# Performance work log

Measured on AMD Instinct MI355X. Metric: run time of the kernel, lower is better.

Reference implementation:

```python
import jax, jax.numpy as jnp
import numpy as np

DC_WZ = 15
ETA = 0.1
RADIUS = DC_WZ // 2  # 7
EPS = 1e-3


def avg_pool2d(x, k, pad):
    # torch F.avg_pool2d default: zero padding, count_include_pad=True -> divide by k*k always
    s = jax.lax.reduce_window(
        x, 0.0, jax.lax.add,
        window_dimensions=(1, 1, k, k),
        window_strides=(1, 1, 1, 1),
        padding=[(0, 0), (0, 0), (pad, pad), (pad, pad)])
    return s / float(k * k)


def min_pool2d_replicate(x, k, pad):
    # replicate (edge) pad then VALID min-pool, matching -max_pool2d(-pad(x, replicate))
    xp = jnp.pad(x, ((0, 0), (0, 0), (pad, pad), (pad, pad)), mode='edge')
    return jax.lax.reduce_window(
        xp, jnp.inf, jax.lax.min,
        window_dimensions=(1, 1, k, k),
        window_strides=(1, 1, 1, 1),
        padding='VALID')


def guided_filter(guide, src, radius, eps=EPS):
    k = 2 * radius + 1
    mean_I = avg_pool2d(guide, k, radius)
    mean_p = avg_pool2d(src, k, radius)
    mean_Ip = avg_pool2d(guide * src, k, radius)
    cov_Ip = mean_Ip - mean_I * mean_p
    mean_II = avg_pool2d(guide * guide, k, radius)
    var_I = mean_II - mean_I * mean_I
    a = cov_Ip / (var_I + eps)
    b = mean_p - a * mean_I
    mean_a = avg_pool2d(a, k, radius)
    mean_b = avg_pool2d(b, k, radius)
    return mean_a * guide + mean_b


def setup_inputs() -> dict:
    key = jax.random.key(0)
    k1, k2 = jax.random.split(key)
    smoky_image = jax.random.uniform(k1, (16, 3, 512, 512), dtype=jnp.float32)
    rho_DNN = jax.random.uniform(k2, (16, 3, 512, 512), dtype=jnp.float32)
    return {"smoky_image": smoky_image, "rho_DNN": rho_DNN}


def reference(smoky_image, rho_DNN):
    # dark channel: per-pixel min over RGB, then 15x15 min-pool with replicate pad
    dc_pixel = jnp.min(smoky_image, axis=-3, keepdims=True)  # [B,1,H,W]
    dc_coarse = min_pool2d_replicate(dc_pixel, DC_WZ, RADIUS)
    guide_I = jnp.mean(smoky_image, axis=-3, keepdims=True)
    dc_refined = guided_filter(guide_I, dc_coarse, RADIUS, EPS)
    dc_refined = jax.lax.stop_gradient(dc_refined)  # torch: no_grad + detach
    dc_rho = (ETA + dc_refined) / (ETA + 1.0) * (1.0 - rho_DNN)
    return smoky_image - dc_rho
```

## Files before the change

### kernel.cpp

```cpp
#include <hip/hip_runtime.h>

#define BATCH 16
#define HH 512
#define WW 512
#define PLANE (HH*WW)

#define LDS_WAIT()   asm volatile("s_waitcnt lgkmcnt(0)" ::: "memory")
#define WAVE_FENCE() asm volatile("" ::: "memory")

__device__ __forceinline__ float bf_lo(unsigned u) {
    union { unsigned u; float f; } c; c.u = u << 16; return c.f;
}
__device__ __forceinline__ float bf_hi(unsigned u) {
    union { unsigned u; float f; } c; c.u = u & 0xFFFF0000u; return c.f;
}
__device__ __forceinline__ unsigned f2bf(float f) {
    union { float f; unsigned u; } c; c.f = f;
    return (c.u + 0x7FFFu + ((c.u >> 16) & 1u)) >> 16;
}
__device__ __forceinline__ unsigned packbf(float x, float y) {
    return f2bf(x) | (f2bf(y) << 16);
}
__device__ __forceinline__ float min3f(float a, float b, float c) {
    return fminf(fminf(a, b), c);
}

#define T1 64
#define HALO 7
#define LW (T1 + 2*HALO)

__global__ __launch_bounds__(256) void k1_guide_minpool(
    const float* __restrict__ smoky, unsigned* __restrict__ gp)
{
    __shared__ float dcp[LW*LW];
    __shared__ float vmn[T1*LW];
    __shared__ unsigned short gsh[T1*T1];
    int nwg = gridDim.x;
    int wg = (blockIdx.x & 7) * (nwg >> 3) + (blockIdx.x >> 3);
    int img  = wg >> 6;
    int tile = wg & 63;
    int y0 = (tile >> 3) * T1;
    int x0 = (tile & 7) * T1;
    int t = threadIdx.x;
    const float* s0 = smoky + (size_t)img * 3 * PLANE;
    unsigned* gpl = gp + (size_t)img * PLANE;

    for (int i = t; i < LW*LW; i += 256) {
        int ly = i / LW, lx = i - ly * LW;
        int iy = y0 - HALO + ly, ix = x0 - HALO + lx;
        int cy = min(max(iy, 0), HH-1);
        int cx = min(max(ix, 0), WW-1);
        const float* bp = s0 + cy * WW + cx;
        float c0 = bp[0], c1 = bp[PLANE], c2 = bp[2*PLANE];
        dcp[i] = min3f(c0, c1, c2);
        if (ly >= HALO && ly < HALO+T1 && lx >= HALO && lx < HALO+T1)
            gsh[(ly-HALO)*T1 + (lx-HALO)] = (unsigned short)f2bf((c0 + c1 + c2) * (1.0f/3.0f));
    }
    __syncthreads();
    for (int i = t; i < T1*LW; i += 256) {
        int r = i / LW, c = i - r * LW;
        const float* q = &dcp[r*LW + c];
        float m = min3f(min3f(min3f(q[0*LW],q[1*LW],q[2*LW]),
                              min3f(q[3*LW],q[4*LW],q[5*LW]),
                              min3f(q[6*LW],q[7*LW],q[8*LW])),
                        min3f(q[9*LW],q[10*LW],q[11*LW]),
                        min3f(q[12*LW],q[13*LW],q[14*LW]));
        vmn[i] = m;
    }
    __syncthreads();
    for (int i = t; i < T1*T1; i += 256) {
        int r = i >> 6, c = i & 63;
        const float* q = &vmn[r*LW + c];
        float m = min3f(min3f(min3f(q[0],q[1],q[2]),
                              min3f(q[3],q[4],q[5]),
                              min3f(q[6],q[7],q[8])),
                        min3f(q[9],q[10],q[11]),
                        min3f(q[12],q[13],q[14]));
        gpl[(y0+r)*WW + x0 + c] = (unsigned)gsh[r*T1+c] | (f2bf(m) << 16);
    }
}

#define RS2 16

#define TSUM15(Q) ( (((Q(0)+Q(1))+(Q(2)+Q(3))) + ((Q(4)+Q(5))+(Q(6)+Q(7)))) \
                  + (((Q(8)+Q(9))+(Q(10)+Q(11))) + ((Q(12)+Q(13))+Q(14))) )

__global__ __launch_bounds__(256) void k2_ab(
    const unsigned* __restrict__ gp, unsigned* __restrict__ abO)
{
    __shared__ float ls[4][4][80];
    int nwg = gridDim.x;
    int wg = (blockIdx.x & 7) * (nwg >> 3) + (blockIdx.x >> 3);
    int w = threadIdx.x >> 6, l = threadIdx.x & 63;
    int gw = wg * 4 + w;
    int img   = gw >> 8;
    int cg    = (gw >> 5) & 7;
    int strip = gw & 31;
    int y0 = strip * RS2;
    int c0 = cg * 64;
    const unsigned* gpP = gp + (size_t)img * PLANE;
    unsigned* abP = abO + (size_t)img * PLANE;

    int col0 = c0 - 7 + l;
    int col1 = c0 + 57 + l;
    bool v0 = (col0 >= 0);
    bool v1 = (l < 14) && (col1 < WW);

    float sI0=0,sII0=0,sP0=0,sIp0=0;
    float sI1=0,sII1=0,sP1=0,sIp1=0;

    auto loadrow = [&](int y, unsigned& u0, unsigned& u1) {
        int yc = min(max(y, 0), HH-1);
        const unsigned* r = gpP + (size_t)yc * WW;
        unsigned a = 0u, b = 0u;
        if (v0) a = r[col0];
        if (v1) b = r[col1];
        bool rv = ((unsigned)y < (unsigned)HH);
        u0 = rv ? a : 0u;
        u1 = rv ? b : 0u;
    };

    for (int r = y0 - 8; r <= y0 + 6; ++r) {
        unsigned u0,u1; loadrow(r, u0,u1);
        float g0=bf_lo(u0), p0=bf_hi(u0), g1=bf_lo(u1), p1=bf_hi(u1);
        sI0+=g0; sII0+=g0*g0; sP0+=p0; sIp0+=g0*p0;
        sI1+=g1; sII1+=g1*g1; sP1+=p1; sIp1+=g1*p1;
    }
    unsigned adA, adB, sbA, sbB;
    loadrow(y0 + 7, adA, adB);
    loadrow(y0 - 8, sbA, sbB);

    float* L = &ls[w][0][0];
    const float inv225 = 1.0f/225.0f;
    for (int y = y0; y < y0 + RS2; ++y) {
        {
            float gA0=bf_lo(adA), pA0=bf_hi(adA), gA1=bf_lo(adB), pA1=bf_hi(adB);
            float gS0=bf_lo(sbA), pS0=bf_hi(sbA), gS1=bf_lo(sbB), pS1=bf_hi(sbB);
            sI0 += gA0-gS0; sII0 += gA0*gA0-gS0*gS0; sP0 += pA0-pS0; sIp0 += gA0*pA0-gS0*pS0;
            sI1 += gA1-gS1; sII1 += gA1*gA1-gS1*gS1; sP1 += pA1-pS1; sIp1 += gA1*pA1-gS1*pS1;
        }
        loadrow(y + 8, adA, adB);
        loadrow(y - 7, sbA, sbB);
        L[l] = sI0; L[80+l] = sII0; L[160+l] = sP0; L[240+l] = sIp0;
        if (l < 14) { L[64+l] = sI1; L[144+l] = sII1; L[224+l] = sP1; L[304+l] = sIp1; }
        LDS_WAIT();
        #define QI(d)  L[l+(d)]
        #define QII(d) L[80+l+(d)]
        #define QP(d)  L[160+l+(d)]
        #define QIp(d) L[240+l+(d)]
        float SI  = TSUM15(QI);
        float SII = TSUM15(QII);
        float SP  = TSUM15(QP);
        float SIp = TSUM15(QIp);
        #undef QI
        #undef QII
        #undef QP
        #undef QIp
        WAVE_FENCE();
        float mI = SI*inv225, mP = SP*inv225;
        float va = (SIp*inv225 - mI*mP) / (SII*inv225 - mI*mI + 1e-3f);
        abP[(size_t)y*WW + c0 + l] = packbf(va, mP - va*mI);
    }
}

__global__ __launch_bounds__(256) void k3_final(
    const unsigned* __restrict__ abI,
    const float* __restrict__ smoky, const float* __restrict__ rho,
    float* __restrict__ out)
{
    __shared__ float ls[4][2][80];
    int nwg = gridDim.x;
    int wg = (blockIdx.x & 7) * (nwg >> 3) + (blockIdx.x >> 3);
    int w = threadIdx.x >> 6, l = threadIdx.x & 63;
    int gw = wg * 4 + w;
    int img   = gw >> 8;
    int cg    = (gw >> 5) & 7;
    int strip = gw & 31;
    int y0 = strip * RS2;
    int c0 = cg * 64;
    const unsigned* abP = abI + (size_t)img * PLANE;
    const float* sP = smoky + (size_t)img * 3 * PLANE;
    const float* rP = rho   + (size_t)img * 3 * PLANE;
    float* oP = out + (size_t)img * 3 * PLANE;

    int col0 = c0 - 7 + l;
    int col1 = c0 + 57 + l;
    bool v0 = (col0 >= 0);
    bool v1 = (l < 14) && (col1 < WW);

    float sa0=0, sb0=0, sa1=0, sb1=0;

    auto loadrow = [&](int y, unsigned& u0, unsigned& u1) {
        int yc = min(max(y, 0), HH-1);
        const unsigned* r = abP + (size_t)yc * WW;
        unsigned a = 0u, b = 0u;
        if (v0) a = r[col0];
        if (v1) b = r[col1];
        bool rv = ((unsigned)y < (unsigned)HH);
        u0 = rv ? a : 0u;
        u1 = rv ? b : 0u;
    };

    for (int r = y0 - 8; r <= y0 + 6; ++r) {
        unsigned u0,u1; loadrow(r, u0,u1);
        sa0 += bf_lo(u0); sb0 += bf_hi(u0);
        sa1 += bf_lo(u1); sb1 += bf_hi(u1);
    }
    unsigned adA, adB, sbA, sbB;
    loadrow(y0 + 7, adA, adB);
    loadrow(y0 - 8, sbA, sbB);

    float es0,es1,es2, er0,er1,er2;
    int yend = y0 + RS2;
    auto loademit = [&](int y) {
        int e = min(y, yend - 1);
        size_t off = (size_t)e*WW + c0 + l;
        es0 = sP[off]; es1 = sP[off+PLANE]; es2 = sP[off+2*PLANE];
        er0 = rP[off]; er1 = rP[off+PLANE]; er2 = rP[off+2*PLANE];
    };
    loademit(y0);

    float* L = &ls[w][0][0];
    const float inv225 = 1.0f/225.0f;
    const float inv11  = 1.0f/1.1f;
    const float third  = 1.0f/3.0f;
    for (int y = y0; y < yend; ++y) {
        sa0 += bf_lo(adA) - bf_lo(sbA);  sb0 += bf_hi(adA) - bf_hi(sbA);
        sa1 += bf_lo(adB) - bf_lo(sbB);  sb1 += bf_hi(adB) - bf_hi(sbB);
        float s0 = es0, s1 = es1, s2 = es2, r0 = er0, r1 = er1, r2 = er2;
        float g = (s0 + s1 + s2) * third;
        loadrow(y + 8, adA, adB);
        loadrow(y - 7, sbA, sbB);
        loademit(y + 1);
        L[l] = sa0; L[80+l] = sb0;
        if (l < 14) { L[64+l] = sa1; L[144+l] = sb1; }
        LDS_WAIT();
        #define QA(d) L[l+(d)]
        #define QB(d) L[80+l+(d)]
        float SA = TSUM15(QA);
        float SB = TSUM15(QB);
        #undef QA
        #undef QB
        WAVE_FENCE();
        float dcr = SA*inv225*g + SB*inv225;
        float f = (0.1f + dcr) * inv11;
        size_t off = (size_t)y*WW + c0 + l;
        oP[off]          = s0 - f*(1.0f - r0);
        oP[off+PLANE]    = s1 - f*(1.0f - r1);
        oP[off+2*PLANE]  = s2 - f*(1.0f - r2);
    }
}

extern "C" void kernel_launch(void* const* d_in, const int* in_sizes, int n_in,
                              void* d_out, int out_size, void* d_ws, size_t ws_size,
                              hipStream_t stream) {
    const float* smoky = (const float*)d_in[0];
    const float* rho   = (const float*)d_in[1];
    float* out = (float*)d_out;
    const size_t P = (size_t)BATCH * PLANE;
    unsigned* gpbuf = (unsigned*)d_ws;
    unsigned* abbuf = (unsigned*)d_ws + P;

    k1_guide_minpool<<<BATCH*64, 256, 0, stream>>>(smoky, gpbuf);
    k2_ab<<<BATCH*64, 256, 0, stream>>>(gpbuf, abbuf);
    k3_final<<<BATCH*64, 256, 0, stream>>>(abbuf, smoky, rho, out);
}
```

Measured before the change: 81.86 us.

## Process two columns per lane with float2 LDS even/odd box-sum sharing

k2 and k3 now give each lane two adjacent columns, so a wave covers 128 columns over 8-row strips instead of 64 columns over 16-row strips. Global loads and stores become 64-bit vectors. Running column sums are stored to LDS as float2 pairs, and the 15-wide horizontal sum for the second column is derived from the first by adding and subtracting one element. This cuts LDS reads, scalar memory instructions and halo overhead per pixel, in exchange for shorter strips that raise the relative cost of the 15-row vertical warm-up and for more registers per lane.

Result: no change. 81.38 us (-0.6%).

```diff
diff --git a/kernel.cpp b/kernel.cpp
--- a/kernel.cpp
+++ b/kernel.cpp
@@ -80,86 +80,112 @@
     }
 }
 
-#define RS2 16
-
-#define TSUM15(Q) ( (((Q(0)+Q(1))+(Q(2)+Q(3))) + ((Q(4)+Q(5))+(Q(6)+Q(7)))) \
-                  + (((Q(8)+Q(9))+(Q(10)+Q(11))) + ((Q(12)+Q(13))+Q(14))) )
+#define RS2 8
 
 __global__ __launch_bounds__(256) void k2_ab(
     const unsigned* __restrict__ gp, unsigned* __restrict__ abO)
 {
-    __shared__ float ls[4][4][80];
+    __shared__ float2 eo[4][4][80];
     int nwg = gridDim.x;
     int wg = (blockIdx.x & 7) * (nwg >> 3) + (blockIdx.x >> 3);
     int w = threadIdx.x >> 6, l = threadIdx.x & 63;
     int gw = wg * 4 + w;
     int img   = gw >> 8;
-    int cg    = (gw >> 5) & 7;
-    int strip = gw & 31;
+    int cg    = (gw >> 6) & 3;
+    int strip = gw & 63;
     int y0 = strip * RS2;
-    int c0 = cg * 64;
+    int c0 = cg * 128;
     const unsigned* gpP = gp + (size_t)img * PLANE;
     unsigned* abP = abO + (size_t)img * PLANE;
 
-    int col0 = c0 - 7 + l;
-    int col1 = c0 + 57 + l;
-    bool v0 = (col0 >= 0);
-    bool v1 = (l < 14) && (col1 < WW);
-
-    float sI0=0,sII0=0,sP0=0,sIp0=0;
-    float sI1=0,sII1=0,sP1=0,sIp1=0;
-
-    auto loadrow = [&](int y, unsigned& u0, unsigned& u1) {
+    int cm = c0 + 2*l;
+    int hj = l & 3;
+    int hcol  = (l < 4) ? (c0 - 8 + 2*hj) : (c0 + 128 + 2*hj);
+    bool hv   = (l < 8) && (hcol >= 0) && (hcol < WW);
+    int hslot = (l < 4) ? hj : (68 + hj);
+
+    float sI[2]={0,0}, sII[2]={0,0}, sPv[2]={0,0}, sIp[2]={0,0};
+    float hI[2]={0,0}, hII[2]={0,0}, hPv[2]={0,0}, hIp[2]={0,0};
+
+    auto loadrow = [&](int y, uint2& um, uint2& uh) {
         int yc = min(max(y, 0), HH-1);
         const unsigned* r = gpP + (size_t)yc * WW;
-        unsigned a = 0u, b = 0u;
-        if (v0) a = r[col0];
-        if (v1) b = r[col1];
+        uint2 a = *reinterpret_cast<const uint2*>(r + cm);
+        uint2 b = make_uint2(0u, 0u);
+        if (hv) b = *reinterpret_cast<const uint2*>(r + hcol);
         bool rv = ((unsigned)y < (unsigned)HH);
-        u0 = rv ? a : 0u;
-        u1 = rv ? b : 0u;
+        um.x = rv ? a.x : 0u;  um.y = rv ? a.y : 0u;
+        uh.x = rv ? b.x : 0u;  uh.y = rv ? b.y : 0u;
     };
 
     for (int r = y0 - 8; r <= y0 + 6; ++r) {
-        unsigned u0,u1; loadrow(r, u0,u1);
-        float g0=bf_lo(u0), p0=bf_hi(u0), g1=bf_lo(u1), p1=bf_hi(u1);
-        sI0+=g0; sII0+=g0*g0; sP0+=p0; sIp0+=g0*p0;
-        sI1+=g1; sII1+=g1*g1; sP1+=p1; sIp1+=g1*p1;
-    }
-    unsigned adA, adB, sbA, sbB;
-    loadrow(y0 + 7, adA, adB);
-    loadrow(y0 - 8, sbA, sbB);
-
-    float* L = &ls[w][0][0];
+        uint2 um, uh; loadrow(r, um, uh);
+        unsigned mm[2]={um.x,um.y}, hh[2]={uh.x,uh.y};
+        #pragma unroll
+        for (int k = 0; k < 2; ++k) {
+            float g=bf_lo(mm[k]), p=bf_hi(mm[k]);
+            sI[k]+=g; sII[k]+=g*g; sPv[k]+=p; sIp[k]+=g*p;
+            float gh=bf_lo(hh[k]), ph=bf_hi(hh[k]);
+            hI[k]+=gh; hII[k]+=gh*gh; hPv[k]+=ph; hIp[k]+=gh*ph;
+        }
+    }
+    uint2 adM, adH, sbM, sbH;
+    loadrow(y0 + 7, adM, adH);
+    loadrow(y0 - 8, sbM, sbH);
+
+    float2* EO = &eo[w][0][0];
     const float inv225 = 1.0f/225.0f;
     for (int y = y0; y < y0 + RS2; ++y) {
         {
-            float gA0=bf_lo(adA), pA0=bf_hi(adA), gA1=bf_lo(adB), pA1=bf_hi(adB);
-            float gS0=bf_lo(sbA), pS0=bf_hi(sbA), gS1=bf_lo(sbB), pS1=bf_hi(sbB);
-            sI0 += gA0-gS0; sII0 += gA0*gA0-gS0*gS0; sP0 += pA0-pS0; sIp0 += gA0*pA0-gS0*pS0;
-            sI1 += gA1-gS1; sII1 += gA1*gA1-gS1*gS1; sP1 += pA1-pS1; sIp1 += gA1*pA1-gS1*pS1;
-        }
-        loadrow(y + 8, adA, adB);
-        loadrow(y - 7, sbA, sbB);
-        L[l] = sI0; L[80+l] = sII0; L[160+l] = sP0; L[240+l] = sIp0;
-        if (l < 14) { L[64+l] = sI1; L[144+l] = sII1; L[224+l] = sP1; L[304+l] = sIp1; }
+            unsigned am[2]={adM.x,adM.y}, sm[2]={sbM.x,sbM.y};
+            unsigned ah[2]={adH.x,adH.y}, sh[2]={sbH.x,sbH.y};
+            #pragma unroll
+            for (int k = 0; k < 2; ++k) {
+                float gA=bf_lo(am[k]), pA=bf_hi(am[k]);
+                float gS=bf_lo(sm[k]), pS=bf_hi(sm[k]);
+                sI[k]+=gA-gS; sII[k]+=gA*gA-gS*gS; sPv[k]+=pA-pS; sIp[k]+=gA*pA-gS*pS;
+                float gAh=bf_lo(ah[k]), pAh=bf_hi(ah[k]);
+                float gSh=bf_lo(sh[k]), pSh=bf_hi(sh[k]);
+                hI[k]+=gAh-gSh; hII[k]+=gAh*gAh-gSh*gSh; hPv[k]+=pAh-pSh; hIp[k]+=gAh*pAh-gSh*pSh;
+            }
+        }
+        loadrow(y + 8, adM, adH);
+        loadrow(y - 7, sbM, sbH);
+        EO[l+4]       = make_float2(sI[0],  sI[1]);
+        EO[80 + l+4]  = make_float2(sII[0], sII[1]);
+        EO[160 + l+4] = make_float2(sPv[0], sPv[1]);
+        EO[240 + l+4] = make_float2(sIp[0], sIp[1]);
+        if (l < 8) {
+            EO[hslot]       = make_float2(hI[0],  hI[1]);
+            EO[80 + hslot]  = make_float2(hII[0], hII[1]);
+            EO[160 + hslot] = make_float2(hPv[0], hPv[1]);
+            EO[240 + hslot] = make_float2(hIp[0], hIp[1]);
+        }
         LDS_WAIT();
-        #define QI(d)  L[l+(d)]
-        #define QII(d) L[80+l+(d)]
-        #define QP(d)  L[160+l+(d)]
-        #define QIp(d) L[240+l+(d)]
-        float SI  = TSUM15(QI);
-        float SII = TSUM15(QII);
-        float SP  = TSUM15(QP);
-        float SIp = TSUM15(QIp);
-        #undef QI
-        #undef QII
-        #undef QP
-        #undef QIp
+        float S0[4], S1[4];
+        #pragma unroll
+        for (int q = 0; q < 4; ++q) {
+            float2 t[9];
+            #pragma unroll
+            for (int m = 0; m < 9; ++m) t[m] = EO[q*80 + l + m];
+            float so = ((t[0].y+t[1].y)+(t[2].y+t[3].y)) + ((t[4].y+t[5].y)+(t[6].y+t[7].y));
+            float se = ((t[1].x+t[2].x)+(t[3].x+t[4].x)) + ((t[5].x+t[6].x)+t[7].x);
+            S0[q] = so + se;
+            S1[q] = S0[q] - t[0].y + t[8].x;
+        }
         WAVE_FENCE();
-        float mI = SI*inv225, mP = SP*inv225;
-        float va = (SIp*inv225 - mI*mP) / (SII*inv225 - mI*mI + 1e-3f);
-        abP[(size_t)y*WW + c0 + l] = packbf(va, mP - va*mI);
+        unsigned pk0, pk1;
+        {
+            float mI = S0[0]*inv225, mP = S0[2]*inv225;
+            float va = (S0[3]*inv225 - mI*mP) / (S0[1]*inv225 - mI*mI + 1e-3f);
+            pk0 = packbf(va, mP - va*mI);
+        }
+        {
+            float mI = S1[0]*inv225, mP = S1[2]*inv225;
+            float va = (S1[3]*inv225 - mI*mP) / (S1[1]*inv225 - mI*mI + 1e-3f);
+            pk1 = packbf(va, mP - va*mI);
+        }
+        *reinterpret_cast<uint2*>(abP + (size_t)y*WW + cm) = make_uint2(pk0, pk1);
     }
 }
 
@@ -168,86 +194,115 @@
     const float* __restrict__ smoky, const float* __restrict__ rho,
     float* __restrict__ out)
 {
-    __shared__ float ls[4][2][80];
+    __shared__ float2 eo[4][2][80];
     int nwg = gridDim.x;
     int wg = (blockIdx.x & 7) * (nwg >> 3) + (blockIdx.x >> 3);
     int w = threadIdx.x >> 6, l = threadIdx.x & 63;
     int gw = wg * 4 + w;
     int img   = gw >> 8;
-    int cg    = (gw >> 5) & 7;
-    int strip = gw & 31;
+    int cg    = (gw >> 6) & 3;
+    int strip = gw & 63;
     int y0 = strip * RS2;
-    int c0 = cg * 64;
+    int c0 = cg * 128;
     const unsigned* abP = abI + (size_t)img * PLANE;
     const float* sP = smoky + (size_t)img * 3 * PLANE;
     const float* rP = rho   + (size_t)img * 3 * PLANE;
     float* oP = out + (size_t)img * 3 * PLANE;
 
-    int col0 = c0 - 7 + l;
-    int col1 = c0 + 57 + l;
-    bool v0 = (col0 >= 0);
-    bool v1 = (l < 14) && (col1 < WW);
-
-    float sa0=0, sb0=0, sa1=0, sb1=0;
-
-    auto loadrow = [&](int y, unsigned& u0, unsigned& u1) {
+    int cm = c0 + 2*l;
+    int hj = l & 3;
+    int hcol  = (l < 4) ? (c0 - 8 + 2*hj) : (c0 + 128 + 2*hj);
+    bool hv   = (l < 8) && (hcol >= 0) && (hcol < WW);
+    int hslot = (l < 4) ? hj : (68 + hj);
+
+    float sa[2]={0,0}, sb[2]={0,0}, ha[2]={0,0}, hb[2]={0,0};
+
+    auto loadrow = [&](int y, uint2& um, uint2& uh) {
         int yc = min(max(y, 0), HH-1);
         const unsigned* r = abP + (size_t)yc * WW;
-        unsigned a = 0u, b = 0u;
-        if (v0) a = r[col0];
-        if (v1) b = r[col1];
+        uint2 a = *reinterpret_cast<const uint2*>(r + cm);
+        uint2 b = make_uint2(0u, 0u);
+        if (hv) b = *reinterpret_cast<const uint2*>(r + hcol);
         bool rv = ((unsigned)y < (unsigned)HH);
-        u0 = rv ? a : 0u;
-        u1 = rv ? b : 0u;
+        um.x = rv ? a.x : 0u;  um.y = rv ? a.y : 0u;
+        uh.x = rv ? b.x : 0u;  uh.y = rv ? b.y : 0u;
     };
 
     for (int r = y0 - 8; r <= y0 + 6; ++r) {
-        unsigned u0,u1; loadrow(r, u0,u1);
-        sa0 += bf_lo(u0); sb0 += bf_hi(u0);
-        sa1 += bf_lo(u1); sb1 += bf_hi(u1);
-    }
-    unsigned adA, adB, sbA, sbB;
-    loadrow(y0 + 7, adA, adB);
-    loadrow(y0 - 8, sbA, sbB);
-
-    float es0,es1,es2, er0,er1,er2;
+        uint2 um, uh; loadrow(r, um, uh);
+        sa[0]+=bf_lo(um.x); sb[0]+=bf_hi(um.x);
+        sa[1]+=bf_lo(um.y); sb[1]+=bf_hi(um.y);
+        ha[0]+=bf_lo(uh.x); hb[0]+=bf_hi(uh.x);
+        ha[1]+=bf_lo(uh.y); hb[1]+=bf_hi(uh.y);
+    }
+    uint2 adM, adH, sbM, sbH;
+    loadrow(y0 + 7, adM, adH);
+    loadrow(y0 - 8, sbM, sbH);
+
+    float2 es0, es1, es2, er0, er1, er2;
     int yend = y0 + RS2;
     auto loademit = [&](int y) {
         int e = min(y, yend - 1);
-        size_t off = (size_t)e*WW + c0 + l;
-        es0 = sP[off]; es1 = sP[off+PLANE]; es2 = sP[off+2*PLANE];
-        er0 = rP[off]; er1 = rP[off+PLANE]; er2 = rP[off+2*PLANE];
+        size_t off = (size_t)e*WW + cm;
+        es0 = *reinterpret_cast<const float2*>(sP + off);
+        es1 = *reinterpret_cast<const float2*>(sP + off + PLANE);
+        es2 = *reinterpret_cast<const float2*>(sP + off + 2*PLANE);
+        er0 = *reinterpret_cast<const float2*>(rP + off);
+        er1 = *reinterpret_cast<const float2*>(rP + off + PLANE);
+        er2 = *reinterpret_cast<const float2*>(rP + off + 2*PLANE);
     };
     loademit(y0);
 
-    float* L = &ls[w][0][0];
+    float2* EO = &eo[w][0][0];
     const float inv225 = 1.0f/225.0f;
     const float inv11  = 1.0f/1.1f;
     const float third  = 1.0f/3.0f;
     for (int y = y0; y < yend; ++y) {
-        sa0 += bf_lo(adA) - bf_lo(sbA);  sb0 += bf_hi(adA) - bf_hi(sbA);
-        sa1 += bf_lo(adB) - bf_lo(sbB);  sb1 += bf_hi(adB) - bf_hi(sbB);
-        float s0 = es0, s1 = es1, s2 = es2, r0 = er0, r1 = er1, r2 = er2;
-        float g = (s0 + s1 + s2) * third;
-        loadrow(y + 8, adA, adB);
-        loadrow(y - 7, sbA, sbB);
+        sa[0] += bf_lo(adM.x) - bf_lo(sbM.x);  sb[0] += bf_hi(adM.x) - bf_hi(sbM.x);
+        sa[1] += bf_lo(adM.y) - bf_lo(sbM.y);  sb[1] += bf_hi(adM.y) - bf_hi(sbM.y);
+        ha[0] += bf_lo(adH.x) - bf_lo(sbH.x);  hb[0] += bf_hi(adH.x) - bf_hi(sbH.x);
+        ha[1] += bf_lo(adH.y) - bf_lo(sbH.y);  hb[1] += bf_hi(adH.y) - bf_hi(sbH.y);
+        float2 cs0 = es0, cs1 = es1, cs2 = es2, cr0 = er0, cr1 = er1, cr2 = er2;
+        loadrow(y + 8, adM, adH);
+        loadrow(y - 7, sbM, sbH);
         loademit(y + 1);
-        L[l] = sa0; L[80+l] = sb0;
-        if (l < 14) { L[64+l] = sa1; L[144+l] = sb1; }
+        EO[l+4]      = make_float2(sa[0], sa[1]);
+        EO[80 + l+4] = make_float2(sb[0], sb[1]);
+        if (l < 8) {
+            EO[hslot]      = make_float2(ha[0], ha[1]);
+            EO[80 + hslot] = make_float2(hb[0], hb[1]);
+        }
         LDS_WAIT();
-        #define QA(d) L[l+(d)]
-        #define QB(d) L[80+l+(d)]
-        float SA = TSUM15(QA);
-        float SB = TSUM15(QB);
-        #undef QA
-        #undef QB
+        float SA0, SA1, SB0, SB1;
+        {
+            float2 t[9];
+            #pragma unroll
+            for (int m = 0; m < 9; ++m) t[m] = EO[l + m];
+            float so = ((t[0].y+t[1].y)+(t[2].y+t[3].y)) + ((t[4].y+t[5].y)+(t[6].y+t[7].y));
+            float se = ((t[1].x+t[2].x)+(t[3].x+t[4].x)) + ((t[5].x+t[6].x)+t[7].x);
+            SA0 = so + se;  SA1 = SA0 - t[0].y + t[8].x;
+        }
+        {
+            float2 t[9];
+            #pragma unroll
+            for (int m = 0; m < 9; ++m) t[m] = EO[80 + l + m];
+            float so = ((t[0].y+t[1].y)+(t[2].y+t[3].y)) + ((t[4].y+t[5].y)+(t[6].y+t[7].y));
+            float se = ((t[1].x+t[2].x)+(t[3].x+t[4].x)) + ((t[5].x+t[6].x)+t[7].x);
+            SB0 = so + se;  SB1 = SB0 - t[0].y + t[8].x;
+        }
         WAVE_FENCE();
-        float dcr = SA*inv225*g + SB*inv225;
-        float f = (0.1f + dcr) * inv11;
-        size_t off = (size_t)y*WW + c0 + l;
-        oP[off]          = s0 - f*(1.0f - r0);
-        oP[off+PLANE]    = s1 - f*(1.0f - r1);
-        oP[off+2*PLANE]  = s2 - f*(1.0f - r2);
+        float g0 = (cs0.x + cs1.x + cs2.x) * third;
+        float g1 = (cs0.y + cs1.y + cs2.y) * third;
+        float f0 = (0.1f + SA0*inv225*g0 + SB0*inv225) * inv11;
+        float f1 = (0.1f + SA1*inv225*g1 + SB1*inv225) * inv11;
+        size_t off = (size_t)y*WW + cm;
+        float2 o0, o1, o2;
+        o0.x = cs0.x - f0*(1.0f - cr0.x);  o0.y = cs0.y - f1*(1.0f - cr0.y);
+        o1.x = cs1.x - f0*(1.0f - cr1.x);  o1.y = cs1.y - f1*(1.0f - cr1.y);
+        o2.x = cs2.x - f0*(1.0f - cr2.x);  o2.y = cs2.y - f1*(1.0f - cr2.y);
+        *reinterpret_cast<float2*>(oP + off)           = o0;
+        *reinterpret_cast<float2*>(oP + off + PLANE)   = o1;
+        *reinterpret_cast<float2*>(oP + off + 2*PLANE) = o2;
     }
 }
 
```

## Fuse a/b computation and final box-filter kernels with an LDS ring buffer

Applied to the files above, without the earlier changes.

Merges the k2 (a,b coefficient) and k3 (mean_a/mean_b plus output) kernels into one kernel. Each wave computes a,b for a widened column halo of 14 pixels per side and a 7-row vertical halo, and keeps them in a 16-row LDS ring buffer that feeds the second running box sum. This removes the intermediate a,b buffer's global write and read plus one launch. In exchange, the halo rows and columns of a,b are recomputed redundantly, there is more LDS traffic, and the emit pipeline gets longer.

After: 122.1 us. 1.49x slower.

```diff
diff --git a/kernel.cpp b/kernel.cpp
--- a/kernel.cpp
+++ b/kernel.cpp
@@ -80,15 +80,17 @@
     }
 }
 
-#define RS2 16
-
-#define TSUM15(Q) ( (((Q(0)+Q(1))+(Q(2)+Q(3))) + ((Q(4)+Q(5))+(Q(6)+Q(7)))) \
-                  + (((Q(8)+Q(9))+(Q(10)+Q(11))) + ((Q(12)+Q(13))+Q(14))) )
-
-__global__ __launch_bounds__(256) void k2_ab(
-    const unsigned* __restrict__ gp, unsigned* __restrict__ abO)
+#define RSF 16
+
+__global__ __launch_bounds__(256) void k23(
+    const unsigned* __restrict__ gp,
+    const float* __restrict__ smoky, const float* __restrict__ rho,
+    float* __restrict__ out)
 {
-    __shared__ float ls[4][4][80];
+    __shared__ float    ex1[4][384];
+    __shared__ unsigned ring[4][16][80];
+    __shared__ float2   ex2[4][80];
+
     int nwg = gridDim.x;
     int wg = (blockIdx.x & 7) * (nwg >> 3) + (blockIdx.x >> 3);
     int w = threadIdx.x >> 6, l = threadIdx.x & 63;
@@ -96,158 +98,138 @@
     int img   = gw >> 8;
     int cg    = (gw >> 5) & 7;
     int strip = gw & 31;
-    int y0 = strip * RS2;
+    int y0 = strip * RSF;
     int c0 = cg * 64;
+
     const unsigned* gpP = gp + (size_t)img * PLANE;
-    unsigned* abP = abO + (size_t)img * PLANE;
-
-    int col0 = c0 - 7 + l;
-    int col1 = c0 + 57 + l;
-    bool v0 = (col0 >= 0);
-    bool v1 = (l < 14) && (col1 < WW);
-
-    float sI0=0,sII0=0,sP0=0,sIp0=0;
-    float sI1=0,sII1=0,sP1=0,sIp1=0;
-
-    auto loadrow = [&](int y, unsigned& u0, unsigned& u1) {
+    const float* sP = smoky + (size_t)img * 3 * PLANE;
+    const float* rP = rho   + (size_t)img * 3 * PLANE;
+    float* oP = out + (size_t)img * 3 * PLANE;
+
+    int colA = c0 - 14 + l;
+    int colB = c0 + 50 + l;
+    bool vA = (colA >= 0);
+    bool vB = (l < 28) && (colB < WW);
+
+    auto loadgp = [&](int y, unsigned& u0, unsigned& u1) {
         int yc = min(max(y, 0), HH-1);
         const unsigned* r = gpP + (size_t)yc * WW;
         unsigned a = 0u, b = 0u;
-        if (v0) a = r[col0];
-        if (v1) b = r[col1];
+        if (vA) a = r[colA];
+        if (vB) b = r[colB];
         bool rv = ((unsigned)y < (unsigned)HH);
         u0 = rv ? a : 0u;
         u1 = rv ? b : 0u;
     };
 
-    for (int r = y0 - 8; r <= y0 + 6; ++r) {
-        unsigned u0,u1; loadrow(r, u0,u1);
+    float sI0=0,sII0=0,sP0=0,sIp0=0;
+    float sI1=0,sII1=0,sP1=0,sIp1=0;
+    float sA0=0,sB0=0;
+    float sA1=0,sB1=0;
+
+    for (int r = y0 - 15; r <= y0 - 1; ++r) {
+        unsigned u0,u1; loadgp(r, u0,u1);
         float g0=bf_lo(u0), p0=bf_hi(u0), g1=bf_lo(u1), p1=bf_hi(u1);
         sI0+=g0; sII0+=g0*g0; sP0+=p0; sIp0+=g0*p0;
         sI1+=g1; sII1+=g1*g1; sP1+=p1; sIp1+=g1*p1;
     }
-    unsigned adA, adB, sbA, sbB;
-    loadrow(y0 + 7, adA, adB);
-    loadrow(y0 - 8, sbA, sbB);
-
-    float* L = &ls[w][0][0];
-    const float inv225 = 1.0f/225.0f;
-    for (int y = y0; y < y0 + RS2; ++y) {
-        {
-            float gA0=bf_lo(adA), pA0=bf_hi(adA), gA1=bf_lo(adB), pA1=bf_hi(adB);
-            float gS0=bf_lo(sbA), pS0=bf_hi(sbA), gS1=bf_lo(sbB), pS1=bf_hi(sbB);
-            sI0 += gA0-gS0; sII0 += gA0*gA0-gS0*gS0; sP0 += pA0-pS0; sIp0 += gA0*pA0-gS0*pS0;
-            sI1 += gA1-gS1; sII1 += gA1*gA1-gS1*gS1; sP1 += pA1-pS1; sIp1 += gA1*pA1-gS1*pS1;
-        }
-        loadrow(y + 8, adA, adB);
-        loadrow(y - 7, sbA, sbB);
-        L[l] = sI0; L[80+l] = sII0; L[160+l] = sP0; L[240+l] = sIp0;
-        if (l < 14) { L[64+l] = sI1; L[144+l] = sII1; L[224+l] = sP1; L[304+l] = sIp1; }
-        LDS_WAIT();
-        #define QI(d)  L[l+(d)]
-        #define QII(d) L[80+l+(d)]
-        #define QP(d)  L[160+l+(d)]
-        #define QIp(d) L[240+l+(d)]
-        float SI  = TSUM15(QI);
-        float SII = TSUM15(QII);
-        float SP  = TSUM15(QP);
-        float SIp = TSUM15(QIp);
-        #undef QI
-        #undef QII
-        #undef QP
-        #undef QIp
-        WAVE_FENCE();
-        float mI = SI*inv225, mP = SP*inv225;
-        float va = (SIp*inv225 - mI*mP) / (SII*inv225 - mI*mI + 1e-3f);
-        abP[(size_t)y*WW + c0 + l] = packbf(va, mP - va*mI);
-    }
-}
-
-__global__ __launch_bounds__(256) void k3_final(
-    const unsigned* __restrict__ abI,
-    const float* __restrict__ smoky, const float* __restrict__ rho,
-    float* __restrict__ out)
-{
-    __shared__ float ls[4][2][80];
-    int nwg = gridDim.x;
-    int wg = (blockIdx.x & 7) * (nwg >> 3) + (blockIdx.x >> 3);
-    int w = threadIdx.x >> 6, l = threadIdx.x & 63;
-    int gw = wg * 4 + w;
-    int img   = gw >> 8;
-    int cg    = (gw >> 5) & 7;
-    int strip = gw & 31;
-    int y0 = strip * RS2;
-    int c0 = cg * 64;
-    const unsigned* abP = abI + (size_t)img * PLANE;
-    const float* sP = smoky + (size_t)img * 3 * PLANE;
-    const float* rP = rho   + (size_t)img * 3 * PLANE;
-    float* oP = out + (size_t)img * 3 * PLANE;
-
-    int col0 = c0 - 7 + l;
-    int col1 = c0 + 57 + l;
-    bool v0 = (col0 >= 0);
-    bool v1 = (l < 14) && (col1 < WW);
-
-    float sa0=0, sb0=0, sa1=0, sb1=0;
-
-    auto loadrow = [&](int y, unsigned& u0, unsigned& u1) {
-        int yc = min(max(y, 0), HH-1);
-        const unsigned* r = abP + (size_t)yc * WW;
-        unsigned a = 0u, b = 0u;
-        if (v0) a = r[col0];
-        if (v1) b = r[col1];
-        bool rv = ((unsigned)y < (unsigned)HH);
-        u0 = rv ? a : 0u;
-        u1 = rv ? b : 0u;
-    };
-
-    for (int r = y0 - 8; r <= y0 + 6; ++r) {
-        unsigned u0,u1; loadrow(r, u0,u1);
-        sa0 += bf_lo(u0); sb0 += bf_hi(u0);
-        sa1 += bf_lo(u1); sb1 += bf_hi(u1);
-    }
-    unsigned adA, adB, sbA, sbB;
-    loadrow(y0 + 7, adA, adB);
-    loadrow(y0 - 8, sbA, sbB);
+    unsigned adG0, adG1, sbG0, sbG1;
+    loadgp(y0,      adG0, adG1);
+    loadgp(y0 - 15, sbG0, sbG1);
 
     float es0,es1,es2, er0,er1,er2;
-    int yend = y0 + RS2;
-    auto loademit = [&](int y) {
-        int e = min(y, yend - 1);
+    auto loademit = [&](int e) {
         size_t off = (size_t)e*WW + c0 + l;
         es0 = sP[off]; es1 = sP[off+PLANE]; es2 = sP[off+2*PLANE];
         er0 = rP[off]; er1 = rP[off+PLANE]; er2 = rP[off+2*PLANE];
     };
     loademit(y0);
 
-    float* L = &ls[w][0][0];
+    float* E1 = &ex1[w][0];
+    unsigned* RG = &ring[w][0][0];
+    float2* E2 = &ex2[w][0];
+
+    auto tsum = [&](const float* p) {
+        return ((((p[0]+p[1])+(p[2]+p[3])) + ((p[4]+p[5])+(p[6]+p[7])))
+              + (((p[8]+p[9])+(p[10]+p[11])) + ((p[12]+p[13])+p[14])));
+    };
+
     const float inv225 = 1.0f/225.0f;
     const float inv11  = 1.0f/1.1f;
     const float third  = 1.0f/3.0f;
-    for (int y = y0; y < yend; ++y) {
-        sa0 += bf_lo(adA) - bf_lo(sbA);  sb0 += bf_hi(adA) - bf_hi(sbA);
-        sa1 += bf_lo(adB) - bf_lo(sbB);  sb1 += bf_hi(adB) - bf_hi(sbB);
-        float s0 = es0, s1 = es1, s2 = es2, r0 = er0, r1 = er1, r2 = er2;
-        float g = (s0 + s1 + s2) * third;
-        loadrow(y + 8, adA, adB);
-        loadrow(y - 7, sbA, sbB);
-        loademit(y + 1);
-        L[l] = sa0; L[80+l] = sb0;
-        if (l < 14) { L[64+l] = sa1; L[144+l] = sb1; }
+
+    for (int t = y0 - 7; t <= y0 + RSF + 6; ++t) {
+        {
+            float gA0=bf_lo(adG0), pA0=bf_hi(adG0), gA1=bf_lo(adG1), pA1=bf_hi(adG1);
+            float gS0=bf_lo(sbG0), pS0=bf_hi(sbG0), gS1=bf_lo(sbG1), pS1=bf_hi(sbG1);
+            sI0 += gA0-gS0; sII0 += gA0*gA0-gS0*gS0; sP0 += pA0-pS0; sIp0 += gA0*pA0-gS0*pS0;
+            sI1 += gA1-gS1; sII1 += gA1*gA1-gS1*gS1; sP1 += pA1-pS1; sIp1 += gA1*pA1-gS1*pS1;
+        }
+        bool emitNow = (t >= y0 + 7);
+        float cs0=es0, cs1=es1, cs2=es2, cr0=er0, cr1=er1, cr2=er2;
+        loadgp(t + 8, adG0, adG1);
+        loadgp(t - 7, sbG0, sbG1);
+        loademit(min(max(t - 6, y0), y0 + RSF - 1));
+        E1[l]       = sI0;  E1[96+l]  = sII0;  E1[192+l]  = sP0;  E1[288+l]  = sIp0;
+        if (l < 28) {
+            E1[64+l] = sI1; E1[160+l] = sII1; E1[256+l] = sP1; E1[352+l] = sIp1;
+        }
         LDS_WAIT();
-        #define QA(d) L[l+(d)]
-        #define QB(d) L[80+l+(d)]
-        float SA = TSUM15(QA);
-        float SB = TSUM15(QB);
-        #undef QA
-        #undef QB
+        float SI0 = tsum(&E1[l]),    SII0 = tsum(&E1[96+l]);
+        float SP0 = tsum(&E1[192+l]), SIp0 = tsum(&E1[288+l]);
+        float SI1=0, SII1_=0, SP1_=0, SIp1_=0;
+        if (l < 14) {
+            SI1   = tsum(&E1[64+l]);  SII1_ = tsum(&E1[160+l]);
+            SP1_  = tsum(&E1[256+l]); SIp1_ = tsum(&E1[352+l]);
+        }
         WAVE_FENCE();
-        float dcr = SA*inv225*g + SB*inv225;
-        float f = (0.1f + dcr) * inv11;
-        size_t off = (size_t)y*WW + c0 + l;
-        oP[off]          = s0 - f*(1.0f - r0);
-        oP[off+PLANE]    = s1 - f*(1.0f - r1);
-        oP[off+2*PLANE]  = s2 - f*(1.0f - r2);
+        bool validT = ((unsigned)t < (unsigned)HH);
+        unsigned pk0 = 0u, pk1 = 0u;
+        {
+            float mI = SI0*inv225, mP = SP0*inv225;
+            float a = (SIp0*inv225 - mI*mP) / (SII0*inv225 - mI*mI + 1e-3f);
+            unsigned pk = packbf(a, mP - a*mI);
+            pk0 = validT ? pk : 0u;
+        }
+        if (l < 14) {
+            float mI = SI1*inv225, mP = SP1_*inv225;
+            float a = (SIp1_*inv225 - mI*mP) / (SII1_*inv225 - mI*mI + 1e-3f);
+            unsigned pk = packbf(a, mP - a*mI);
+            pk1 = validT ? pk : 0u;
+        }
+        unsigned old0 = RG[((t+1)&15)*80 + l];
+        unsigned old1 = (l < 14) ? RG[((t+1)&15)*80 + 64 + l] : 0u;
+        RG[(t&15)*80 + l] = pk0;
+        if (l < 14) RG[(t&15)*80 + 64 + l] = pk1;
+        bool subOK = (t - 15 >= y0 - 7);
+        float oa0 = subOK ? bf_lo(old0) : 0.f, ob0 = subOK ? bf_hi(old0) : 0.f;
+        float oa1 = subOK ? bf_lo(old1) : 0.f, ob1 = subOK ? bf_hi(old1) : 0.f;
+        sA0 += bf_lo(pk0) - oa0;  sB0 += bf_hi(pk0) - ob0;
+        sA1 += bf_lo(pk1) - oa1;  sB1 += bf_hi(pk1) - ob1;
+        WAVE_FENCE();
+        if (emitNow) {
+            E2[l] = make_float2(sA0, sB0);
+            if (l < 14) E2[64+l] = make_float2(sA1, sB1);
+            LDS_WAIT();
+            float SA, SB;
+            {
+                float2 u0=E2[l],   u1=E2[l+1],  u2=E2[l+2],  u3=E2[l+3],  u4=E2[l+4];
+                float2 u5=E2[l+5], u6=E2[l+6],  u7=E2[l+7],  u8=E2[l+8],  u9=E2[l+9];
+                float2 ua=E2[l+10],ub=E2[l+11], uc=E2[l+12], ud=E2[l+13], ue=E2[l+14];
+                SA = ((((u0.x+u1.x)+(u2.x+u3.x)) + ((u4.x+u5.x)+(u6.x+u7.x)))
+                   + (((u8.x+u9.x)+(ua.x+ub.x)) + ((uc.x+ud.x)+ue.x)));
+                SB = ((((u0.y+u1.y)+(u2.y+u3.y)) + ((u4.y+u5.y)+(u6.y+u7.y)))
+                   + (((u8.y+u9.y)+(ua.y+ub.y)) + ((uc.y+ud.y)+ue.y)));
+            }
+            WAVE_FENCE();
+            float g = (cs0 + cs1 + cs2) * third;
+            float f = (0.1f + SA*inv225*g + SB*inv225) * inv11;
+            int e = t - 7;
+            size_t off = (size_t)e*WW + c0 + l;
+            oP[off]          = cs0 - f*(1.0f - cr0);
+            oP[off+PLANE]    = cs1 - f*(1.0f - cr1);
+            oP[off+2*PLANE]  = cs2 - f*(1.0f - cr2);
+        }
     }
 }
 
@@ -257,11 +239,8 @@
     const float* smoky = (const float*)d_in[0];
     const float* rho   = (const float*)d_in[1];
     float* out = (float*)d_out;
-    const size_t P = (size_t)BATCH * PLANE;
     unsigned* gpbuf = (unsigned*)d_ws;
-    unsigned* abbuf = (unsigned*)d_ws + P;
 
     k1_guide_minpool<<<BATCH*64, 256, 0, stream>>>(smoky, gpbuf);
-    k2_ab<<<BATCH*64, 256, 0, stream>>>(gpbuf, abbuf);
-    k3_final<<<BATCH*64, 256, 0, stream>>>(abbuf, smoky, rho, out);
-}
+    k23<<<BATCH*64, 256, 0, stream>>>(gpbuf, smoky, rho, out);
+}
```
